# Kernel optimization log

Measured on AMD Instinct MI355X. Metric: run time of the kernel, lower is better.

The kernel has to match this reference:

```python
import jax, jax.numpy as jnp
import numpy as np

SCALE = 4.0  # VeRA scale hyperparameter


def setup_inputs() -> dict:
    key = jax.random.key(0)
    ks = jax.random.split(key, 7)
    T, IN, OUT, R = 8192, 4096, 4096, 256
    return {
        "x": jax.random.normal(ks[0], (T, IN), dtype=jnp.float32),
        "base_weight": jax.random.normal(ks[1], (OUT, IN), dtype=jnp.float32) * 0.02,
        "base_bias": jax.random.normal(ks[2], (OUT,), dtype=jnp.float32) * 0.02,
        "vera_random_A": jax.random.normal(ks[3], (R, IN), dtype=jnp.float32) * (1.0 / np.sqrt(IN)),
        "vera_random_B": jax.random.normal(ks[4], (OUT, R), dtype=jnp.float32) * (1.0 / np.sqrt(R)),
        "vera_d": jax.random.normal(ks[5], (R,), dtype=jnp.float32) * 0.01,
        "vera_b": 0.1 * jnp.ones((OUT,), dtype=jnp.float32),
    }


def reference(x, base_weight, base_bias, vera_random_A, vera_random_B, vera_d, vera_b):
    # delta_W = scale * diag(vera_b) @ B @ diag(vera_d) @ A  -> row/col scaling, no diag matmuls
    # shapes: B (out, r), A (r, in), delta (out, in)
    delta = SCALE * jnp.einsum("or,ri->oi", vera_b[:, None] * vera_random_B, vera_d[:, None] * vera_random_A)
    # linear: y = x @ (W + delta)^T + bias
    return x @ (base_weight + delta).T + base_bias
```

## Files before the change

### kernel.cpp

```cpp
#include <hip/hip_runtime.h>


typedef __attribute__((ext_vector_type(8))) short short8;
typedef __attribute__((ext_vector_type(4))) float f32x4;

__device__ __forceinline__ unsigned short f2bf(float f) {
  union { float f; unsigned int u; } c; c.f = f;
  unsigned int u = c.u;
  unsigned int r = (u + 0x7fffu + ((u >> 16) & 1u)) >> 16;
  return (unsigned short)r;
}

__device__ __forceinline__ void gl2lds16(const unsigned short* g, unsigned short* l) {
  __builtin_amdgcn_global_load_lds(
      (const __attribute__((address_space(1))) unsigned int*)g,
      (__attribute__((address_space(3))) unsigned int*)l, 16, 0, 0);
}

__global__ __launch_bounds__(256) void k_pre(const float* __restrict__ x,
                                             unsigned short* __restrict__ xb,
                                             const float* __restrict__ Bv,
                                             const float* __restrict__ Av,
                                             const float* __restrict__ dv,
                                             const float* __restrict__ bv,
                                             unsigned short* __restrict__ Bd,
                                             unsigned short* __restrict__ AbT) {
  __shared__ float tl[32][33];
  const int blk = blockIdx.x;
  const int tid = threadIdx.x;
  if (blk < 8192) {
#pragma unroll
    for (int s = 0; s < 4; ++s) {
      int i = blk * 1024 + s * 256 + tid;
      const float4 v = ((const float4*)x)[i];
      union { unsigned short u[4]; unsigned long long ll; } o;
      o.u[0] = f2bf(v.x); o.u[1] = f2bf(v.y); o.u[2] = f2bf(v.z); o.u[3] = f2bf(v.w);
      ((unsigned long long*)xb)[i] = o.ll;
    }
  } else if (blk < 12288) {
    int idx = (blk - 8192) * 256 + tid;
    int o = idx >> 8, r = idx & 255;
    Bd[idx] = f2bf(4.0f * bv[o] * Bv[idx] * dv[r]);
  } else {
    int blk2 = blk - 12288;
    int ti = blk2 >> 3;
    int tr = blk2 & 7;
#pragma unroll
    for (int s = 0; s < 4; ++s) {
      int r = tr * 32 + s * 8 + (tid >> 5);
      int i = ti * 32 + (tid & 31);
      tl[s * 8 + (tid >> 5)][tid & 31] = Av[(size_t)r * 4096 + i];
    }
    __syncthreads();
#pragma unroll
    for (int s = 0; s < 4; ++s) {
      int iloc = s * 8 + (tid >> 5);
      int rloc = tid & 31;
      AbT[(size_t)(ti * 32 + iloc) * 256 + tr * 32 + rloc] = f2bf(tl[rloc][iloc]);
    }
  }
}

template <int FOLD>
__global__ __launch_bounds__(512, 2) void gemm256(const unsigned short* __restrict__ Amat,
                                                  const unsigned short* __restrict__ Bmat,
                                                  int K, int N, int NBX,
                                                  const float* __restrict__ extra,
                                                  float* __restrict__ outF,
                                                  unsigned short* __restrict__ outB) {
  __shared__ __align__(16) unsigned short As[2 * 2 * 8192];
  __shared__ __align__(16) unsigned short Bs[2 * 2 * 8192];

  const int tid  = threadIdx.x;
  const int lane = tid & 63;
  const int wave = tid >> 6;
  const int wm   = wave >> 2;
  const int wn   = wave & 3;
  const int quad = lane >> 4;
  const int m16  = lane & 15;
  const int qsl  = quad ^ ((m16 >> 1) & 3);

  const int nwg  = gridDim.x;
  const int cpx  = nwg >> 3;
  const int wgid = (blockIdx.x & 7) * cpx + (blockIdx.x >> 3);
  const int bx   = wgid % NBX;
  const int by   = wgid / NBX;
  const int blockM = by * 256;
  const int blockN = bx * 256;

  const int srow = tid >> 2;
  const int sq8  = ((tid & 3) ^ ((tid >> 3) & 3)) * 8;
  const size_t aB0 = (size_t)(blockM + srow) * K + sq8;
  const size_t aB1 = aB0 + (size_t)128 * K;
  const size_t bB0 = (size_t)(blockN + srow) * K + sq8;
  const size_t bB1 = bB0 + (size_t)128 * K;

  const short8* Asv = (const short8*)As;
  const short8* Bsv = (const short8*)Bs;
  const int aRd = wm * 512 + m16 * 4 + qsl;
  const int bRd = wn * 256 + m16 * 4 + qsl;

  f32x4 acc[8][4];
#pragma unroll
  for (int i = 0; i < 8; ++i)
#pragma unroll
    for (int j = 0; j < 4; ++j) acc[i][j] = (f32x4){0.f, 0.f, 0.f, 0.f};

  short8 afr[4];
  short8 bfr[8];

#define VM4()  asm volatile("s_waitcnt vmcnt(4)" ::: "memory")
#define VM0()  asm volatile("s_waitcnt vmcnt(0)" ::: "memory")
#define NOPW() ((void)0)

#define ISSUE_A(bufi, kh, koff) do {                                         \
    unsigned short* d_ = As + ((bufi) * 2 + (kh)) * 8192 + tid * 8;          \
    gl2lds16(Amat + aB0 + (koff) + (kh) * 32, d_);                           \
    gl2lds16(Amat + aB1 + (koff) + (kh) * 32, d_ + 4096);                    \
  } while (0)

#define ISSUE_B(bufi, kh, koff) do {                                         \
    unsigned short* d_ = Bs + ((bufi) * 2 + (kh)) * 8192 + tid * 8;          \
    gl2lds16(Bmat + bB0 + (koff) + (kh) * 32, d_);                           \
    gl2lds16(Bmat + bB1 + (koff) + (kh) * 32, d_ + 4096);                    \
  } while (0)

#define RD_B8(Bb) do {                                                       \
    _Pragma("unroll") for (int kh = 0; kh < 2; ++kh)                         \
    _Pragma("unroll") for (int nt = 0; nt < 4; ++nt)                         \
      bfr[kh * 4 + nt] = Bsv[((Bb) * 2 + kh) * 1024 + bRd + nt * 64];        \
  } while (0)

#define RD_A4(Bb, q) do {                                                    \
    _Pragma("unroll") for (int kh = 0; kh < 2; ++kh)                         \
    _Pragma("unroll") for (int mt = 0; mt < 2; ++mt)                         \
      afr[kh * 2 + mt] =                                                     \
          Asv[((Bb) * 2 + kh) * 1024 + aRd + (q) * 128 + mt * 64];           \
  } while (0)

#define MM16(q) do {                                                         \
    _Pragma("unroll") for (int kh = 0; kh < 2; ++kh)                         \
    _Pragma("unroll") for (int mt = 0; mt < 2; ++mt)                         \
    _Pragma("unroll") for (int nt = 0; nt < 4; ++nt)                         \
      acc[(q) * 2 + mt][nt] = __builtin_amdgcn_mfma_f32_16x16x32_bf16(       \
          afr[kh * 2 + mt], bfr[kh * 4 + nt], acc[(q) * 2 + mt][nt], 0, 0, 0);\
  } while (0)

#define PH(Bb, q, STAGE, WAITOPT) do {                                       \
    if ((q) == 0) { RD_B8(Bb); }                                             \
    RD_A4(Bb, q);                                                            \
    STAGE;                                                                   \
    WAITOPT;                                                                 \
    asm volatile("s_barrier" ::: "memory");                                  \
    asm volatile("s_waitcnt lgkmcnt(0)" ::: "memory");                       \
    __builtin_amdgcn_sched_barrier(0);                                       \
    __builtin_amdgcn_s_setprio(1);                                           \
    MM16(q);                                                                 \
    __builtin_amdgcn_s_setprio(0);                                           \
    __builtin_amdgcn_sched_barrier(0);                                       \
    asm volatile("s_barrier" ::: "memory");                                  \
  } while (0)

  ISSUE_A(0, 0, (size_t)0);  ISSUE_A(0, 1, (size_t)0);
  ISSUE_B(0, 0, (size_t)0);  ISSUE_B(0, 1, (size_t)0);
  ISSUE_B(1, 0, (size_t)64); ISSUE_B(1, 1, (size_t)64);
  VM4();
  asm volatile("s_barrier" ::: "memory");

  const int NT = K >> 6;
  const int NI = NT >> 1;
  size_t ko = 0;
  for (int i = 0; i < NI - 1; ++i) {
    PH(0, 0, ISSUE_A(1, 0, ko + 64),  NOPW());
    PH(0, 1, ISSUE_A(1, 1, ko + 64),  NOPW());
    PH(0, 2, ISSUE_B(0, 0, ko + 128), NOPW());
    PH(0, 3, ISSUE_B(0, 1, ko + 128), VM4());
    PH(1, 0, ISSUE_A(0, 0, ko + 128), NOPW());
    PH(1, 1, ISSUE_A(0, 1, ko + 128), NOPW());
    PH(1, 2, ISSUE_B(1, 0, ko + 192), NOPW());
    PH(1, 3, ISSUE_B(1, 1, ko + 192), VM4());
    ko += 128;
  }
  PH(0, 0, ISSUE_A(1, 0, ko + 64), NOPW());
  PH(0, 1, ISSUE_A(1, 1, ko + 64), NOPW());
  PH(0, 2, NOPW(), NOPW());
  PH(0, 3, NOPW(), VM0());
  PH(1, 0, NOPW(), NOPW());
  PH(1, 1, NOPW(), NOPW());
  PH(1, 2, NOPW(), NOPW());
  PH(1, 3, NOPW(), NOPW());

#undef VM4
#undef VM0
#undef NOPW
#undef ISSUE_A
#undef ISSUE_B
#undef RD_B8
#undef RD_A4
#undef MM16
#undef PH

#pragma unroll
  for (int mt = 0; mt < 8; ++mt) {
    const int row0 = blockM + wm * 128 + mt * 16 + quad * 4;
#pragma unroll
    for (int nt = 0; nt < 4; ++nt) {
      const int col = blockN + wn * 64 + nt * 16 + m16;
      f32x4 v = acc[mt][nt];
      if (FOLD) {
#pragma unroll
        for (int r = 0; r < 4; ++r) {
          size_t o = (size_t)(row0 + r) * N + col;
          outB[o] = f2bf(extra[o] + v[r]);
        }
      } else {
        const float bb = extra[col];
#pragma unroll
        for (int r = 0; r < 4; ++r) {
          size_t o = (size_t)(row0 + r) * N + col;
          outF[o] = v[r] + bb;
        }
      }
    }
  }
}

extern "C" void kernel_launch(void* const* d_in, const int* in_sizes, int n_in,
                              void* d_out, int out_size, void* d_ws, size_t ws_size,
                              hipStream_t stream) {
  const float* x    = (const float*)d_in[0];
  const float* W    = (const float*)d_in[1];
  const float* bias = (const float*)d_in[2];
  const float* A    = (const float*)d_in[3];
  const float* B    = (const float*)d_in[4];
  const float* dv   = (const float*)d_in[5];
  const float* bv   = (const float*)d_in[6];
  float* out = (float*)d_out;

  char* ws = (char*)d_ws;
  unsigned short* xb  = (unsigned short*)ws;
  unsigned short* Wc  = (unsigned short*)(ws + (size_t)(64 << 20));
  unsigned short* Bd  = (unsigned short*)(ws + (size_t)(96 << 20));
  unsigned short* AbT = (unsigned short*)(ws + (size_t)(98 << 20));

  hipLaunchKernelGGL(k_pre, dim3(13312), dim3(256), 0, stream,
                     x, xb, B, A, dv, bv, Bd, AbT);
  hipLaunchKernelGGL((gemm256<1>), dim3(256), dim3(512), 0, stream,
                     Bd, AbT, 256, 4096, 16, W, (float*)nullptr, Wc);
  hipLaunchKernelGGL((gemm256<0>), dim3(512), dim3(512), 0, stream,
                     xb, Wc, 4096, 4096, 16, bias, out, (unsigned short*)nullptr);
}
```

Measured before the change: 553.5 us.

## Double-buffer LDS fragment registers and halve barriers in GEMM main loop

```diff
diff --git a/kernel.cpp b/kernel.cpp
--- a/kernel.cpp
+++ b/kernel.cpp
@@ -106,12 +106,16 @@
 #pragma unroll
     for (int j = 0; j < 4; ++j) acc[i][j] = (f32x4){0.f, 0.f, 0.f, 0.f};
 
-  short8 afr[4];
-  short8 bfr[8];
-
-#define VM4()  asm volatile("s_waitcnt vmcnt(4)" ::: "memory")
-#define VM0()  asm volatile("s_waitcnt vmcnt(0)" ::: "memory")
-#define NOPW() ((void)0)
+  short8 afr0[4], afr1[4];
+  short8 bfr0[8], bfr1[8];
+
+#define BAR()   asm volatile("s_barrier" ::: "memory")
+#define LGKM0() asm volatile("s_waitcnt lgkmcnt(0)" ::: "memory")
+#define VMW4()  asm volatile("s_waitcnt vmcnt(4)" ::: "memory")
+#define VMW0()  asm volatile("s_waitcnt vmcnt(0)" ::: "memory")
+#define SBAR()  __builtin_amdgcn_sched_barrier(0)
+#define PRIO1() __builtin_amdgcn_s_setprio(1)
+#define PRIO0() __builtin_amdgcn_s_setprio(0)
 
 #define ISSUE_A(bufi, kh, koff) do {                                         \
     unsigned short* d_ = As + ((bufi) * 2 + (kh)) * 8192 + tid * 8;          \
@@ -125,80 +129,111 @@
     gl2lds16(Bmat + bB1 + (koff) + (kh) * 32, d_ + 4096);                    \
   } while (0)
 
-#define RD_B8(Bb) do {                                                       \
+#define RDB8(dst, Bb) do {                                                   \
     _Pragma("unroll") for (int kh = 0; kh < 2; ++kh)                         \
     _Pragma("unroll") for (int nt = 0; nt < 4; ++nt)                         \
-      bfr[kh * 4 + nt] = Bsv[((Bb) * 2 + kh) * 1024 + bRd + nt * 64];        \
-  } while (0)
-
-#define RD_A4(Bb, q) do {                                                    \
+      dst[kh * 4 + nt] = Bsv[((Bb) * 2 + kh) * 1024 + bRd + nt * 64];        \
+  } while (0)
+
+#define RDA4(dst, Bb, q) do {                                                \
     _Pragma("unroll") for (int kh = 0; kh < 2; ++kh)                         \
     _Pragma("unroll") for (int mt = 0; mt < 2; ++mt)                         \
-      afr[kh * 2 + mt] =                                                     \
+      dst[kh * 2 + mt] =                                                     \
           Asv[((Bb) * 2 + kh) * 1024 + aRd + (q) * 128 + mt * 64];           \
   } while (0)
 
-#define MM16(q) do {                                                         \
+#define MM16(q, AF, BF) do {                                                 \
+    PRIO1();                                                                 \
     _Pragma("unroll") for (int kh = 0; kh < 2; ++kh)                         \
     _Pragma("unroll") for (int mt = 0; mt < 2; ++mt)                         \
     _Pragma("unroll") for (int nt = 0; nt < 4; ++nt)                         \
       acc[(q) * 2 + mt][nt] = __builtin_amdgcn_mfma_f32_16x16x32_bf16(       \
-          afr[kh * 2 + mt], bfr[kh * 4 + nt], acc[(q) * 2 + mt][nt], 0, 0, 0);\
-  } while (0)
-
-#define PH(Bb, q, STAGE, WAITOPT) do {                                       \
-    if ((q) == 0) { RD_B8(Bb); }                                             \
-    RD_A4(Bb, q);                                                            \
-    STAGE;                                                                   \
-    WAITOPT;                                                                 \
-    asm volatile("s_barrier" ::: "memory");                                  \
-    asm volatile("s_waitcnt lgkmcnt(0)" ::: "memory");                       \
-    __builtin_amdgcn_sched_barrier(0);                                       \
-    __builtin_amdgcn_s_setprio(1);                                           \
-    MM16(q);                                                                 \
-    __builtin_amdgcn_s_setprio(0);                                           \
-    __builtin_amdgcn_sched_barrier(0);                                       \
-    asm volatile("s_barrier" ::: "memory");                                  \
+          AF[kh * 2 + mt], BF[kh * 4 + nt], acc[(q) * 2 + mt][nt], 0, 0, 0); \
+    PRIO0();                                                                 \
   } while (0)
 
   ISSUE_A(0, 0, (size_t)0);  ISSUE_A(0, 1, (size_t)0);
   ISSUE_B(0, 0, (size_t)0);  ISSUE_B(0, 1, (size_t)0);
   ISSUE_B(1, 0, (size_t)64); ISSUE_B(1, 1, (size_t)64);
-  VM4();
-  asm volatile("s_barrier" ::: "memory");
+  VMW4();
 
   const int NT = K >> 6;
   const int NI = NT >> 1;
   size_t ko = 0;
   for (int i = 0; i < NI - 1; ++i) {
-    PH(0, 0, ISSUE_A(1, 0, ko + 64),  NOPW());
-    PH(0, 1, ISSUE_A(1, 1, ko + 64),  NOPW());
-    PH(0, 2, ISSUE_B(0, 0, ko + 128), NOPW());
-    PH(0, 3, ISSUE_B(0, 1, ko + 128), VM4());
-    PH(1, 0, ISSUE_A(0, 0, ko + 128), NOPW());
-    PH(1, 1, ISSUE_A(0, 1, ko + 128), NOPW());
-    PH(1, 2, ISSUE_B(1, 0, ko + 192), NOPW());
-    PH(1, 3, ISSUE_B(1, 1, ko + 192), VM4());
+    BAR();
+    RDB8(bfr0, 0); RDA4(afr0, 0, 0);
+    ISSUE_A(1, 0, ko + 64); ISSUE_A(1, 1, ko + 64);
+    LGKM0(); SBAR();
+    MM16(0, afr0, bfr0);
+    RDA4(afr1, 0, 1);
+    BAR(); ISSUE_B(0, 0, ko + 128); LGKM0(); SBAR();
+    MM16(1, afr1, bfr0);
+    RDA4(afr0, 0, 2);
+    BAR(); ISSUE_B(0, 1, ko + 128); LGKM0(); SBAR();
+    MM16(2, afr0, bfr0);
+    RDA4(afr1, 0, 3);
+    BAR(); LGKM0(); SBAR();
+    MM16(3, afr1, bfr0);
+    VMW4();
+    BAR();
+    RDB8(bfr1, 1); RDA4(afr0, 1, 0);
+    ISSUE_A(0, 0, ko + 128); ISSUE_A(0, 1, ko + 128);
+    LGKM0(); SBAR();
+    MM16(0, afr0, bfr1);
+    RDA4(afr1, 1, 1);
+    BAR(); LGKM0(); SBAR();
+    MM16(1, afr1, bfr1);
+    RDA4(afr0, 1, 2);
+    BAR(); ISSUE_B(1, 0, ko + 192); LGKM0(); SBAR();
+    MM16(2, afr0, bfr1);
+    RDA4(afr1, 1, 3);
+    BAR(); ISSUE_B(1, 1, ko + 192); LGKM0(); SBAR();
+    MM16(3, afr1, bfr1);
+    VMW4();
     ko += 128;
   }
-  PH(0, 0, ISSUE_A(1, 0, ko + 64), NOPW());
-  PH(0, 1, ISSUE_A(1, 1, ko + 64), NOPW());
-  PH(0, 2, NOPW(), NOPW());
-  PH(0, 3, NOPW(), VM0());
-  PH(1, 0, NOPW(), NOPW());
-  PH(1, 1, NOPW(), NOPW());
-  PH(1, 2, NOPW(), NOPW());
-  PH(1, 3, NOPW(), NOPW());
-
-#undef VM4
-#undef VM0
-#undef NOPW
+  BAR();
+  RDB8(bfr0, 0); RDA4(afr0, 0, 0);
+  ISSUE_A(1, 0, ko + 64); ISSUE_A(1, 1, ko + 64);
+  LGKM0(); SBAR();
+  MM16(0, afr0, bfr0);
+  RDA4(afr1, 0, 1);
+  BAR(); LGKM0(); SBAR();
+  MM16(1, afr1, bfr0);
+  RDA4(afr0, 0, 2);
+  BAR(); LGKM0(); SBAR();
+  MM16(2, afr0, bfr0);
+  RDA4(afr1, 0, 3);
+  BAR(); LGKM0(); SBAR();
+  MM16(3, afr1, bfr0);
+  VMW0();
+  BAR();
+  RDB8(bfr1, 1); RDA4(afr0, 1, 0);
+  LGKM0(); SBAR();
+  MM16(0, afr0, bfr1);
+  RDA4(afr1, 1, 1);
+  BAR(); LGKM0(); SBAR();
+  MM16(1, afr1, bfr1);
+  RDA4(afr0, 1, 2);
+  BAR(); LGKM0(); SBAR();
+  MM16(2, afr0, bfr1);
+  RDA4(afr1, 1, 3);
+  BAR(); LGKM0(); SBAR();
+  MM16(3, afr1, bfr1);
+
+#undef BAR
+#undef LGKM0
+#undef VMW4
+#undef VMW0
+#undef SBAR
+#undef PRIO1
+#undef PRIO0
 #undef ISSUE_A
 #undef ISSUE_B
-#undef RD_B8
-#undef RD_A4
+#undef RDB8
+#undef RDA4
 #undef MM16
-#undef PH
 
 #pragma unroll
   for (int mt = 0; mt < 8; ++mt) {
```

New measurement: 540.8 us. 2.3% less time.
